# Optimization experiments

Measured on AMD Instinct MI355X. Metric: run time of the kernel, lower is better.

Reference implementation:

```python
import jax, jax.numpy as jnp
import numpy as np

B, C, H, W = 4, 256, 256, 256   # batch, channels, height, width
NH, HD, P, G = 8, 32, 8, 32     # num_heads, head_dim, patch_size, groupnorm groups
EPS = 1e-6


def setup_inputs() -> dict:
    key = jax.random.key(0)
    ks = jax.random.split(key, 6)
    w = lambda k: jax.random.normal(k, (C, C), jnp.float32) * 0.02
    return {
        "q": jax.random.normal(ks[0], (B, C, H, W), jnp.float32),
        "gn_w": jnp.ones((C,), jnp.float32),
        "gn_b": jnp.zeros((C,), jnp.float32),
        "q_w": w(ks[1]), "q_b": jnp.zeros((C,), jnp.float32),
        "k_w": w(ks[2]), "k_b": jnp.zeros((C,), jnp.float32),
        "v_w": w(ks[3]), "v_b": jnp.zeros((C,), jnp.float32),
        "o_w": w(ks[4]), "o_b": jnp.zeros((C,), jnp.float32),
    }


def group_norm(x, w, b):
    bsz, c, h, wd = x.shape
    xg = x.reshape(bsz, G, c // G, h, wd)
    mu = xg.mean(axis=(2, 3, 4), keepdims=True)
    var = xg.var(axis=(2, 3, 4), keepdims=True)
    xg = (xg - mu) * jax.lax.rsqrt(var + EPS)
    return xg.reshape(bsz, c, h, wd) * w[None, :, None, None] + b[None, :, None, None]


def conv1x1(x, w, b):
    return jnp.einsum('bchw,oc->bohw', x, w) + b[None, :, None, None]


def reference(q, gn_w, gn_b, q_w, q_b, k_w, k_b, v_w, v_b, o_w, o_b):
    q_in = q
    xn = group_norm(q, gn_w, gn_b)           # v is None -> v = normalized q
    qq = conv1x1(xn, q_w, q_b)
    kk = conv1x1(xn, k_w, k_b)
    vv = conv1x1(xn, v_w, v_b)
    b_, c, h, w = qq.shape
    hp, wp = h // P, w // P

    def win(t):  # (b,C,h,w) -> (b,NH, n_windows, P*P, HD)
        t = t.reshape(b_, NH, HD, hp, P, wp, P)
        t = t.transpose(0, 1, 2, 3, 5, 4, 6)        # (b,NH,HD,hp,wp,P,P)
        t = jnp.moveaxis(t, 2, -1)                  # (b,NH,hp,wp,P,P,HD)
        return t.reshape(b_, NH, hp * wp, P * P, HD)

    qw_, kw_, vw_ = win(qq), win(kk), win(vv)
    scale = HD ** -0.5
    attn = jax.nn.softmax(jnp.einsum('bhnqd,bhnkd->bhnqk', qw_, kw_) * scale, axis=-1)
    out = jnp.einsum('bhnqk,bhnkd->bhnqd', attn, vw_)

    # inverse reshuffle: (b,NH,n,P*P,HD) -> (b,C,h,w)
    out = jnp.moveaxis(out, -1, 2).reshape(b_, c, hp, wp, P, P)
    out = out.transpose(0, 1, 2, 4, 3, 5).reshape(b_, c, h, w)
    out = conv1x1(out, o_w, o_b)
    return (out + q_in) * np.float32(2 ** -0.5)
```

## Files before the change

### kernel.cpp

```cpp
#include <hip/hip_runtime.h>
#include <hip/hip_bf16.h>
#include <stdint.h>

#define B_   4
#define C_   256
#define HW_  65536
#define NH_  8
#define HD_  32
#define G_   32
#define CPG_ 8

typedef __bf16 bf16x8 __attribute__((ext_vector_type(8)));
typedef float  f32x4  __attribute__((ext_vector_type(4)));

__device__ __forceinline__ unsigned short f2bf(float f) {
  union { float f; unsigned u; } v; v.f = f;
  unsigned r = v.u + 0x7fffu + ((v.u >> 16) & 1u);
  return (unsigned short)(r >> 16);
}

#define GL16(gp, lp) __builtin_amdgcn_global_load_lds( \
    (const __attribute__((address_space(1))) void*)(gp), \
    (__attribute__((address_space(3))) void*)(lp), 16, 0, 0)

__global__ void gn_partial(const float* __restrict__ x, float* __restrict__ part) {
  int chunk = blockIdx.x, g = blockIdx.y, b = blockIdx.z;
  const float* p = x + ((size_t)b * C_ + g * CPG_) * HW_ + (size_t)chunk * 65536;
  int t = threadIdx.x;
  float s1 = 0.f, s2 = 0.f;
  for (int it = 0; it < 64; ++it) {
    float4 v = reinterpret_cast<const float4*>(p)[it * 256 + t];
    s1 += v.x + v.y + v.z + v.w;
    s2 += v.x * v.x + v.y * v.y + v.z * v.z + v.w * v.w;
  }
  for (int off = 32; off; off >>= 1) {
    s1 += __shfl_xor(s1, off, 64);
    s2 += __shfl_xor(s2, off, 64);
  }
  __shared__ float ls1[4], ls2[4];
  int wv = t >> 6;
  if ((t & 63) == 0) { ls1[wv] = s1; ls2[wv] = s2; }
  __syncthreads();
  if (t == 0) {
    float a = ls1[0] + ls1[1] + ls1[2] + ls1[3];
    float c = ls2[0] + ls2[1] + ls2[2] + ls2[3];
    int gi = (b * G_ + g) * 8 + chunk;
    part[gi * 2] = a; part[gi * 2 + 1] = c;
  }
}

__global__ void gn_finalize(const float* __restrict__ part,
                            const float* __restrict__ gn_w, const float* __restrict__ gn_b,
                            float* __restrict__ A, float* __restrict__ D) {
  int b = blockIdx.x, c = threadIdx.x;
  int g = c >> 3;
  float s1 = 0.f, s2 = 0.f;
  for (int k = 0; k < 8; ++k) {
    s1 += part[((b * G_ + g) * 8 + k) * 2];
    s2 += part[((b * G_ + g) * 8 + k) * 2 + 1];
  }
  const float invN = 1.0f / (float)(CPG_ * HW_);
  float mu = s1 * invN;
  float var = s2 * invN - mu * mu;
  float rstd = rsqrtf(var + 1e-6f);
  float a = rstd * gn_w[c];
  A[b * C_ + c] = a;
  D[b * C_ + c] = gn_b[c] - mu * a;
}

__global__ void pack_weights(const float* __restrict__ qw, const float* __restrict__ kw,
                             const float* __restrict__ vw, const float* __restrict__ ow,
                             unsigned short* __restrict__ Wall, unsigned short* __restrict__ Wo) {
  int idx = blockIdx.x * 256 + threadIdx.x;
  if (idx < 196608) {
    int o = idx >> 8, c = idx & 255;
    float v = (o < 256) ? qw[o * 256 + c]
            : (o < 512) ? kw[(o - 256) * 256 + c]
                        : vw[(o - 512) * 256 + c];
    Wall[idx] = f2bf(v);
  } else {
    int j = idx - 196608;
    Wo[j] = f2bf(ow[j]);
  }
}

__global__ void norm_transpose(const float* __restrict__ x, const float* __restrict__ A,
                               const float* __restrict__ D, unsigned short* __restrict__ xn) {
  __shared__ float Ts[64][65];
  __shared__ float As[64], Ds[64];
  int hw0 = blockIdx.x * 64, c0 = blockIdx.y * 64, b = blockIdx.z;
  int t = threadIdx.x;
  if (t < 64) { As[t] = A[b * C_ + c0 + t]; Ds[t] = D[b * C_ + c0 + t]; }
  const float* xb = x + (size_t)b * C_ * HW_;
  for (int it = 0; it < 4; ++it) {
    int idx = it * 256 + t;
    int ch = idx >> 4, p4 = idx & 15;
    float4 v = *reinterpret_cast<const float4*>(xb + (size_t)(c0 + ch) * HW_ + hw0 + p4 * 4);
    Ts[ch][p4 * 4 + 0] = v.x; Ts[ch][p4 * 4 + 1] = v.y;
    Ts[ch][p4 * 4 + 2] = v.z; Ts[ch][p4 * 4 + 3] = v.w;
  }
  __syncthreads();
  unsigned short* outb = xn + ((size_t)b * HW_ + hw0) * C_ + c0;
  for (int it = 0; it < 2; ++it) {
    int idx = it * 256 + t;
    int px = idx >> 3, ck = (idx & 7) * 8;
    union { uint4 u; unsigned short s[8]; } tmp;
    for (int j = 0; j < 8; ++j) {
      float v = Ts[ck + j][px] * As[ck + j] + Ds[ck + j];
      tmp.s[j] = f2bf(v);
    }
    *reinterpret_cast<uint4*>(outb + (size_t)px * C_ + ck) = tmp.u;
  }
}

__global__ __launch_bounds__(256, 2) void qkv_gemm(
    const unsigned short* __restrict__ Wall, const unsigned short* __restrict__ xn,
    const float* __restrict__ qb, const float* __restrict__ kb, const float* __restrict__ vb,
    unsigned short* __restrict__ qkv) {
  __shared__ __align__(16) unsigned short As[128 * 32];
  __shared__ __align__(16) unsigned short Bs[128 * 32];
  int mt = blockIdx.x, nt = blockIdx.y, b = blockIdx.z;
  int m0 = mt * 128, n0 = nt * 128;
  int t = threadIdx.x;
  int wv = t >> 6, lane = t & 63;
  int lanelo = lane & 15, quad = lane >> 4;
  const unsigned short* xb = xn + (size_t)b * HW_ * C_;
  f32x4 acc[4][4];
  for (int i = 0; i < 4; ++i)
    for (int j = 0; j < 4; ++j) acc[i][j] = f32x4{0.f, 0.f, 0.f, 0.f};
  int row_in = lane >> 2;
  int kcol = (lane & 3) * 8;
  int wm = wv & 1, wn = wv >> 1;
  for (int kt = 0; kt < 8; ++kt) {
    int k0 = kt * 32;
    for (int j = 0; j < 2; ++j) {
      int r = wv * 32 + j * 16 + row_in;
      GL16(Wall + (size_t)(m0 + r) * 256 + k0 + kcol, &As[(wv * 2 + j) * 512]);
      GL16(xb + (size_t)(n0 + r) * 256 + k0 + kcol, &Bs[(wv * 2 + j) * 512]);
    }
    __syncthreads();
    bf16x8 af[4], bff[4];
    for (int i = 0; i < 4; ++i) {
      af[i]  = *reinterpret_cast<const bf16x8*>(&As[(wm * 64 + i * 16 + lanelo) * 32 + quad * 8]);
      bff[i] = *reinterpret_cast<const bf16x8*>(&Bs[(wn * 64 + i * 16 + lanelo) * 32 + quad * 8]);
    }
    for (int i = 0; i < 4; ++i)
      for (int j = 0; j < 4; ++j)
        acc[i][j] = __builtin_amdgcn_mfma_f32_16x16x32_bf16(af[i], bff[j], acc[i][j], 0, 0, 0);
    __syncthreads();
  }
  for (int i = 0; i < 4; ++i) {
    int o_base = m0 + wm * 64 + i * 16 + quad * 4;
    for (int j = 0; j < 4; ++j) {
      int n = n0 + wn * 64 + j * 16 + lanelo;
      for (int r = 0; r < 4; ++r) {
        int o = o_base + r;
        float bias = (o < 256) ? qb[o] : (o < 512) ? kb[o - 256] : vb[o - 512];
        qkv[((size_t)b * 768 + o) * HW_ + n] = f2bf(acc[i][j][r] + bias);
      }
    }
  }
}

__global__ __launch_bounds__(64) void attn_kernel(const unsigned short* __restrict__ qkv,
                                                  unsigned short* __restrict__ attn) {
  __shared__ __align__(16) unsigned short Qs[64 * 40];
  __shared__ __align__(16) unsigned short Ks[64 * 40];
  __shared__ __align__(16) unsigned short Vt[32 * 72];
  __shared__ __align__(16) unsigned short Ps[16 * 72];
  __shared__ __align__(16) unsigned short Os[16 * 40];
  int idx = blockIdx.x;
  int wp = idx & 31, head = (idx >> 5) & 7, hp = (idx >> 8) & 31, b = idx >> 13;
  int lane = threadIdx.x;
  int lanelo = lane & 15, quad = lane >> 4;
  size_t base = ((size_t)b * 768 + head * 32) * HW_ + (size_t)(hp * 8) * 256 + wp * 8;
  for (int it = 0; it < 4; ++it) {
    int id = it * 64 + lane;
    int d = id & 31, r = id >> 5;
    size_t goff = (size_t)d * HW_ + (size_t)r * 256;
    union { uint4 u; unsigned short s[8]; } q, k, v;
    q.u = *reinterpret_cast<const uint4*>(qkv + base + goff);
    k.u = *reinterpret_cast<const uint4*>(qkv + base + (size_t)256 * HW_ + goff);
    v.u = *reinterpret_cast<const uint4*>(qkv + base + (size_t)512 * HW_ + goff);
    for (int j = 0; j < 8; ++j) {
      Qs[(r * 8 + j) * 40 + d] = q.s[j];
      Ks[(r * 8 + j) * 40 + d] = k.s[j];
    }
    *reinterpret_cast<uint4*>(&Vt[d * 72 + r * 8]) = v.u;
  }
  __syncthreads();
  bf16x8 kf[4], vf0[2], vf1[2];
  for (int ni = 0; ni < 4; ++ni)
    kf[ni] = *reinterpret_cast<const bf16x8*>(&Ks[(ni * 16 + lanelo) * 40 + quad * 8]);
  for (int n2 = 0; n2 < 2; ++n2) {
    vf0[n2] = *reinterpret_cast<const bf16x8*>(&Vt[(n2 * 16 + lanelo) * 72 + quad * 8]);
    vf1[n2] = *reinterpret_cast<const bf16x8*>(&Vt[(n2 * 16 + lanelo) * 72 + 32 + quad * 8]);
  }
  const float scale = 0.17677669529663687f;
  const f32x4 zero = {0.f, 0.f, 0.f, 0.f};
  unsigned short* attb = attn + (size_t)b * HW_ * C_ + head * 32;
  for (int mi = 0; mi < 4; ++mi) {
    bf16x8 qf = *reinterpret_cast<const bf16x8*>(&Qs[(mi * 16 + lanelo) * 40 + quad * 8]);
    f32x4 s[4];
    for (int ni = 0; ni < 4; ++ni)
      s[ni] = __builtin_amdgcn_mfma_f32_16x16x32_bf16(qf, kf[ni], zero, 0, 0, 0);
    for (int r = 0; r < 4; ++r) {
      float mx = fmaxf(fmaxf(s[0][r], s[1][r]), fmaxf(s[2][r], s[3][r])) * scale;
      for (int off = 1; off < 16; off <<= 1) mx = fmaxf(mx, __shfl_xor(mx, off, 16));
      float p[4], sum = 0.f;
      for (int ni = 0; ni < 4; ++ni) { p[ni] = __expf(s[ni][r] * scale - mx); sum += p[ni]; }
      for (int off = 1; off < 16; off <<= 1) sum += __shfl_xor(sum, off, 16);
      float inv = 1.0f / sum;
      for (int ni = 0; ni < 4; ++ni)
        Ps[(quad * 4 + r) * 72 + ni * 16 + lanelo] = f2bf(p[ni] * inv);
    }
    __syncthreads();
    bf16x8 p0 = *reinterpret_cast<const bf16x8*>(&Ps[lanelo * 72 + quad * 8]);
    bf16x8 p1 = *reinterpret_cast<const bf16x8*>(&Ps[lanelo * 72 + 32 + quad * 8]);
    f32x4 o0 = __builtin_amdgcn_mfma_f32_16x16x32_bf16(p0, vf0[0], zero, 0, 0, 0);
    o0 = __builtin_amdgcn_mfma_f32_16x16x32_bf16(p1, vf1[0], o0, 0, 0, 0);
    f32x4 o1 = __builtin_amdgcn_mfma_f32_16x16x32_bf16(p0, vf0[1], zero, 0, 0, 0);
    o1 = __builtin_amdgcn_mfma_f32_16x16x32_bf16(p1, vf1[1], o1, 0, 0, 0);
    for (int r = 0; r < 4; ++r) {
      Os[(quad * 4 + r) * 40 + lanelo] = f2bf(o0[r]);
      Os[(quad * 4 + r) * 40 + 16 + lanelo] = f2bf(o1[r]);
    }
    __syncthreads();
    {
      int tok = lane >> 2, part = lane & 3;
      uint4 vv = *reinterpret_cast<const uint4*>(&Os[tok * 40 + part * 8]);
      int gt = mi * 16 + tok;
      int pix = (hp * 8 + (gt >> 3)) * 256 + wp * 8 + (gt & 7);
      *reinterpret_cast<uint4*>(attb + (size_t)pix * C_ + part * 8) = vv;
    }
    __syncthreads();
  }
}

__global__ __launch_bounds__(256, 2) void oproj_gemm(
    const unsigned short* __restrict__ Wo, const unsigned short* __restrict__ attn,
    const float* __restrict__ ob, const float* __restrict__ qin, float* __restrict__ out) {
  __shared__ __align__(16) unsigned short As[128 * 32];
  __shared__ __align__(16) unsigned short Bs[128 * 32];
  int mt = blockIdx.x, nt = blockIdx.y, b = blockIdx.z;
  int m0 = mt * 128, n0 = nt * 128;
  int t = threadIdx.x;
  int wv = t >> 6, lane = t & 63;
  int lanelo = lane & 15, quad = lane >> 4;
  const unsigned short* xb = attn + (size_t)b * HW_ * C_;
  f32x4 acc[4][4];
  for (int i = 0; i < 4; ++i)
    for (int j = 0; j < 4; ++j) acc[i][j] = f32x4{0.f, 0.f, 0.f, 0.f};
  int row_in = lane >> 2;
  int kcol = (lane & 3) * 8;
  int wm = wv & 1, wn = wv >> 1;
  for (int kt = 0; kt < 8; ++kt) {
    int k0 = kt * 32;
    for (int j = 0; j < 2; ++j) {
      int r = wv * 32 + j * 16 + row_in;
      GL16(Wo + (size_t)(m0 + r) * 256 + k0 + kcol, &As[(wv * 2 + j) * 512]);
      GL16(xb + (size_t)(n0 + r) * 256 + k0 + kcol, &Bs[(wv * 2 + j) * 512]);
    }
    __syncthreads();
    bf16x8 af[4], bff[4];
    for (int i = 0; i < 4; ++i) {
      af[i]  = *reinterpret_cast<const bf16x8*>(&As[(wm * 64 + i * 16 + lanelo) * 32 + quad * 8]);
      bff[i] = *reinterpret_cast<const bf16x8*>(&Bs[(wn * 64 + i * 16 + lanelo) * 32 + quad * 8]);
    }
    for (int i = 0; i < 4; ++i)
      for (int j = 0; j < 4; ++j)
        acc[i][j] = __builtin_amdgcn_mfma_f32_16x16x32_bf16(af[i], bff[j], acc[i][j], 0, 0, 0);
    __syncthreads();
  }
  const float rs2 = 0.7071067811865476f;
  for (int i = 0; i < 4; ++i) {
    int o_base = m0 + wm * 64 + i * 16 + quad * 4;
    for (int j = 0; j < 4; ++j) {
      int n = n0 + wn * 64 + j * 16 + lanelo;
      for (int r = 0; r < 4; ++r) {
        int o = o_base + r;
        size_t off = ((size_t)b * C_ + o) * HW_ + n;
        out[off] = (acc[i][j][r] + ob[o] + qin[off]) * rs2;
      }
    }
  }
}

extern "C" void kernel_launch(void* const* d_in, const int* in_sizes, int n_in,
                              void* d_out, int out_size, void* d_ws, size_t ws_size,
                              hipStream_t stream) {
  const float* x    = (const float*)d_in[0];
  const float* gn_w = (const float*)d_in[1];
  const float* gn_b = (const float*)d_in[2];
  const float* q_w  = (const float*)d_in[3];
  const float* q_b  = (const float*)d_in[4];
  const float* k_w  = (const float*)d_in[5];
  const float* k_b  = (const float*)d_in[6];
  const float* v_w  = (const float*)d_in[7];
  const float* v_b  = (const float*)d_in[8];
  const float* o_w  = (const float*)d_in[9];
  const float* o_b  = (const float*)d_in[10];
  float* out = (float*)d_out;
  char* ws = (char*)d_ws;

  float* part = (float*)(ws + 0);
  float* A    = (float*)(ws + 8192);
  float* D    = (float*)(ws + 12288);
  unsigned short* Wall = (unsigned short*)(ws + 16384);
  unsigned short* Wo   = (unsigned short*)(ws + 16384 + 393216);
  unsigned short* xn   = (unsigned short*)(ws + ((size_t)1 << 20));
  unsigned short* qkv  = (unsigned short*)(ws + ((size_t)1 << 20) + ((size_t)128 << 20));
  unsigned short* attn = xn;

  gn_partial<<<dim3(8, 32, 4), 256, 0, stream>>>(x, part);
  gn_finalize<<<dim3(4), 256, 0, stream>>>(part, gn_w, gn_b, A, D);
  pack_weights<<<dim3(1024), 256, 0, stream>>>(q_w, k_w, v_w, o_w, Wall, Wo);
  norm_transpose<<<dim3(1024, 4, 4), 256, 0, stream>>>(x, A, D, xn);
  qkv_gemm<<<dim3(6, 512, 4), 256, 0, stream>>>(Wall, xn, q_b, k_b, v_b, qkv);
  attn_kernel<<<dim3(32768), 64, 0, stream>>>(qkv, attn);
  oproj_gemm<<<dim3(2, 512, 4), 256, 0, stream>>>(Wo, attn, o_b, x, out);
}
```

Before: 1.414 ms.

## Store normalized activations in window-major order and swizzle attention LDS

The normalize-transpose kernel now writes pixels in window-major token order, so the QKV output is contiguous per 8x8 window. The attention kernel then loads each window's 64 tokens per channel contiguously, uses an XOR swizzle on Q/K shared-memory columns to reduce bank conflicts, and writes its output contiguously. The output projection permutes its B-tile rows and epilogue pixel mapping so stores land back in NCHW. This trades strided window gathers for contiguous loads, at the cost of more scattered writes in norm_transpose and the final epilogue.

```diff
diff --git a/kernel.cpp b/kernel.cpp
--- a/kernel.cpp
+++ b/kernel.cpp
@@ -22,6 +22,7 @@
 #define GL16(gp, lp) __builtin_amdgcn_global_load_lds( \
     (const __attribute__((address_space(1))) void*)(gp), \
     (__attribute__((address_space(3))) void*)(lp), 16, 0, 0)
+
 
 __global__ void gn_partial(const float* __restrict__ x, float* __restrict__ part) {
   int chunk = blockIdx.x, g = blockIdx.y, b = blockIdx.z;
@@ -100,7 +101,9 @@
     Ts[ch][p4 * 4 + 2] = v.z; Ts[ch][p4 * 4 + 3] = v.w;
   }
   __syncthreads();
-  unsigned short* outb = xn + ((size_t)b * HW_ + hw0) * C_ + c0;
+  int h = hw0 >> 8, w0 = hw0 & 255;
+  int nbase = ((h >> 3) * 32) * 64 + ((h & 7) * 8);
+  unsigned short* outb = xn + (size_t)b * HW_ * C_ + c0;
   for (int it = 0; it < 2; ++it) {
     int idx = it * 256 + t;
     int px = idx >> 3, ck = (idx & 7) * 8;
@@ -109,7 +112,9 @@
       float v = Ts[ck + j][px] * As[ck + j] + Ds[ck + j];
       tmp.s[j] = f2bf(v);
     }
-    *reinterpret_cast<uint4*>(outb + (size_t)px * C_ + ck) = tmp.u;
+    int w = w0 + px;
+    int np = nbase + ((w >> 3) << 6) + (w & 7);
+    *reinterpret_cast<uint4*>(outb + (size_t)np * C_ + ck) = tmp.u;
   }
 }
 
@@ -170,37 +175,47 @@
   __shared__ __align__(16) unsigned short Ps[16 * 72];
   __shared__ __align__(16) unsigned short Os[16 * 40];
   int idx = blockIdx.x;
-  int wp = idx & 31, head = (idx >> 5) & 7, hp = (idx >> 8) & 31, b = idx >> 13;
+  int win = idx & 1023, head = (idx >> 10) & 7, b = idx >> 13;
   int lane = threadIdx.x;
   int lanelo = lane & 15, quad = lane >> 4;
-  size_t base = ((size_t)b * 768 + head * 32) * HW_ + (size_t)(hp * 8) * 256 + wp * 8;
+  size_t base = ((size_t)b * 768 + head * 32) * HW_ + (size_t)win * 64;
   for (int it = 0; it < 4; ++it) {
     int id = it * 64 + lane;
-    int d = id & 31, r = id >> 5;
-    size_t goff = (size_t)d * HW_ + (size_t)r * 256;
+    int d = id >> 3, m = id & 7;
+    int t8 = m * 8;
+    size_t goff = (size_t)d * HW_ + t8;
     union { uint4 u; unsigned short s[8]; } q, k, v;
     q.u = *reinterpret_cast<const uint4*>(qkv + base + goff);
     k.u = *reinterpret_cast<const uint4*>(qkv + base + (size_t)256 * HW_ + goff);
     v.u = *reinterpret_cast<const uint4*>(qkv + base + (size_t)512 * HW_ + goff);
+    int col = ((it ^ (m & 3)) << 3) | (d & 7);
     for (int j = 0; j < 8; ++j) {
-      Qs[(r * 8 + j) * 40 + d] = q.s[j];
-      Ks[(r * 8 + j) * 40 + d] = k.s[j];
-    }
-    *reinterpret_cast<uint4*>(&Vt[d * 72 + r * 8]) = v.u;
+      Qs[(t8 + j) * 40 + col] = q.s[j];
+      Ks[(t8 + j) * 40 + col] = k.s[j];
+    }
+    *reinterpret_cast<uint4*>(&Vt[d * 72 + t8]) = v.u;
   }
   __syncthreads();
   bf16x8 kf[4], vf0[2], vf1[2];
-  for (int ni = 0; ni < 4; ++ni)
-    kf[ni] = *reinterpret_cast<const bf16x8*>(&Ks[(ni * 16 + lanelo) * 40 + quad * 8]);
+  for (int ni = 0; ni < 4; ++ni) {
+    int row = ni * 16 + lanelo;
+    int g = quad ^ ((row >> 3) & 3);
+    kf[ni] = *reinterpret_cast<const bf16x8*>(&Ks[row * 40 + g * 8]);
+  }
   for (int n2 = 0; n2 < 2; ++n2) {
     vf0[n2] = *reinterpret_cast<const bf16x8*>(&Vt[(n2 * 16 + lanelo) * 72 + quad * 8]);
     vf1[n2] = *reinterpret_cast<const bf16x8*>(&Vt[(n2 * 16 + lanelo) * 72 + 32 + quad * 8]);
   }
   const float scale = 0.17677669529663687f;
   const f32x4 zero = {0.f, 0.f, 0.f, 0.f};
-  unsigned short* attb = attn + (size_t)b * HW_ * C_ + head * 32;
+  unsigned short* attb = attn + ((size_t)b * HW_ + (size_t)win * 64) * C_ + head * 32;
   for (int mi = 0; mi < 4; ++mi) {
-    bf16x8 qf = *reinterpret_cast<const bf16x8*>(&Qs[(mi * 16 + lanelo) * 40 + quad * 8]);
+    bf16x8 qf;
+    {
+      int row = mi * 16 + lanelo;
+      int g = quad ^ ((row >> 3) & 3);
+      qf = *reinterpret_cast<const bf16x8*>(&Qs[row * 40 + g * 8]);
+    }
     f32x4 s[4];
     for (int ni = 0; ni < 4; ++ni)
       s[ni] = __builtin_amdgcn_mfma_f32_16x16x32_bf16(qf, kf[ni], zero, 0, 0, 0);
@@ -230,8 +245,7 @@
       int tok = lane >> 2, part = lane & 3;
       uint4 vv = *reinterpret_cast<const uint4*>(&Os[tok * 40 + part * 8]);
       int gt = mi * 16 + tok;
-      int pix = (hp * 8 + (gt >> 3)) * 256 + wp * 8 + (gt & 7);
-      *reinterpret_cast<uint4*>(attb + (size_t)pix * C_ + part * 8) = vv;
+      *reinterpret_cast<uint4*>(attb + (size_t)gt * C_ + part * 8) = vv;
     }
     __syncthreads();
   }
@@ -258,8 +272,9 @@
     int k0 = kt * 32;
     for (int j = 0; j < 2; ++j) {
       int r = wv * 32 + j * 16 + row_in;
+      int rp = (r & 7) | (((r >> 3) & 1) << 6) | (((r >> 4) & 7) << 3);
       GL16(Wo + (size_t)(m0 + r) * 256 + k0 + kcol, &As[(wv * 2 + j) * 512]);
-      GL16(xb + (size_t)(n0 + r) * 256 + k0 + kcol, &Bs[(wv * 2 + j) * 512]);
+      GL16(xb + (size_t)(n0 + rp) * 256 + k0 + kcol, &Bs[(wv * 2 + j) * 512]);
     }
     __syncthreads();
     bf16x8 af[4], bff[4];
@@ -276,10 +291,14 @@
   for (int i = 0; i < 4; ++i) {
     int o_base = m0 + wm * 64 + i * 16 + quad * 4;
     for (int j = 0; j < 4; ++j) {
-      int n = n0 + wn * 64 + j * 16 + lanelo;
+      int f = wn * 64 + j * 16 + lanelo;
+      int fp = (f & 7) | (((f >> 3) & 1) << 6) | (((f >> 4) & 7) << 3);
+      int np = n0 + fp;
+      int win = np >> 6, tok = np & 63;
+      int pix = ((win >> 5) * 8 + (tok >> 3)) * 256 + ((win & 31) * 8) + (tok & 7);
       for (int r = 0; r < 4; ++r) {
         int o = o_base + r;
-        size_t off = ((size_t)b * C_ + o) * HW_ + n;
+        size_t off = ((size_t)b * C_ + o) * HW_ + pix;
         out[off] = (acc[i][j][r] + ob[o] + qin[off]) * rs2;
       }
     }
```

Result: faster. 1.193 ms (-15.6%).
